# Kernel tuning notes

Measured on AMD Instinct MI355X. Metric: run time of the kernel, lower is better.

Reference implementation:

```python
import jax, jax.numpy as jnp
import numpy as np

D, B, E, O = 8, 16, 2048, 2048  # delays, batch, pre, post


def setup_inputs() -> dict:
    key = jax.random.key(0)
    k_w, k_mask, k_xd, k_dm, k_ws, k_sp = jax.random.split(key, 6)
    # W = connectivity mask * magnitudes (sparse non-negative weights, buffer wmax folded in)
    conn = jax.random.bernoulli(k_mask, 0.1, (E, O)).astype(jnp.float32)
    W = jax.random.uniform(k_w, (E, O), dtype=jnp.float32) * 0.02 * conn
    # Delayed presynaptic spikes: sparse binary
    Xd = jax.random.bernoulli(k_xd, 0.02, (D, B, E)).astype(jnp.float32)
    # delaymap: binary (delay, pre, post) routing map, typically ~1 active delay per synapse
    delaymap = jax.random.bernoulli(k_dm, 0.125, (D, E, O)).astype(jnp.float32)
    # STP modulation (output of shortterm module, before the +1 offset)
    Wshort = (jax.random.uniform(k_ws, (D, B, E), dtype=jnp.float32) - 0.5) * 0.4
    # Per-presynaptic-neuron signs in {-1,+1}, stored as int
    signs_pre = jax.random.randint(k_sp, (E,), 0, 2, dtype=jnp.int32)
    return {"W": W, "Xd": Xd, "delaymap": delaymap, "Wshort": Wshort,
            "signs_pre": signs_pre}


def reference(W, Xd, delaymap, Wshort, signs_pre):
    # align_signs(): signs = signs_pre broadcast over post, zeroed where W <= 0
    s = (2 * signs_pre - 1).astype(W.dtype)  # map {0,1} -> {-1,+1}
    signs = jnp.where(W > 0, s[:, None], jnp.zeros((), W.dtype))  # (E, O)
    Ws = signs * W  # signed weights 'eo'
    # has_STP path: I = einsum('eo,dbe,deo,dbe->bo', W, Xd, delaymap, Wshort+1)
    I = jnp.einsum('eo,dbe,deo,dbe->bo', Ws, Xd, delaymap, Wshort + 1.0)
    return I
```

## Files before the change

### kernel.cpp

```cpp
#include <hip/hip_runtime.h>


constexpr int D = 8, B = 16, E = 2048, O = 2048;
constexpr int DB = D * B;
constexpr int OTILE = 1024;
constexpr int THREADS2 = OTILE / 4;
constexpr int ESPLIT = 2;

struct Entry { int e; float c; };

__global__ __launch_bounds__(256) void build_lists(
    const float* __restrict__ Xd, const float* __restrict__ Wshort,
    const int* __restrict__ signs, int* __restrict__ counts,
    Entry* __restrict__ entries)
{
    const int db = blockIdx.x;
    __shared__ int cnt;
    if (threadIdx.x == 0) cnt = 0;
    __syncthreads();
    const float* xrow = Xd + (size_t)db * E;
    const float* wsr  = Wshort + (size_t)db * E;
    Entry* out = entries + (size_t)db * E;
    for (int e = threadIdx.x; e < E; e += blockDim.x) {
        float x = xrow[e];
        if (x != 0.0f) {
            float s = (float)(2 * signs[e] - 1);
            float c = x * s * (1.0f + wsr[e]);
            int slot = atomicAdd(&cnt, 1);
            out[slot].e = e;
            out[slot].c = c;
        }
    }
    __syncthreads();
    if (threadIdx.x == 0) counts[db] = cnt;
}

__global__ __launch_bounds__(THREADS2) void accum(
    const float* __restrict__ W, const float* __restrict__ dm,
    const int* __restrict__ counts, const Entry* __restrict__ entries,
    float* __restrict__ Iout)
{
    const int tile = blockIdx.x;
    const int part = blockIdx.y;
    const int db   = blockIdx.z;
    const int d = db / B;
    const int b = db % B;
    const int o0 = tile * OTILE + (int)threadIdx.x * 4;

    const int n = counts[db];
    const Entry* __restrict__ lst = entries + (size_t)db * E;

    float4 acc = make_float4(0.f, 0.f, 0.f, 0.f);
    #pragma unroll 2
    for (int i = part; i < n; i += ESPLIT) {
        Entry en = lst[i];
        const float4 w = *(const float4*)(W  + (size_t)en.e * O + o0);
        const float4 m = *(const float4*)(dm + ((size_t)d * E + en.e) * O + o0);
        acc.x += en.c * w.x * m.x;
        acc.y += en.c * w.y * m.y;
        acc.z += en.c * w.z * m.z;
        acc.w += en.c * w.w * m.w;
    }

    float* orow = Iout + (size_t)b * O + o0;
#if defined(__HIP_DEVICE_COMPILE__)
    unsafeAtomicAdd(orow + 0, acc.x);
    unsafeAtomicAdd(orow + 1, acc.y);
    unsafeAtomicAdd(orow + 2, acc.z);
    unsafeAtomicAdd(orow + 3, acc.w);
#endif
}

extern "C" void kernel_launch(void* const* d_in, const int* in_sizes, int n_in,
                              void* d_out, int out_size, void* d_ws, size_t ws_size,
                              hipStream_t stream) {
    const float* W     = (const float*)d_in[0];
    const float* Xd    = (const float*)d_in[1];
    const float* dm    = (const float*)d_in[2];
    const float* Wsh   = (const float*)d_in[3];
    const int*   signs = (const int*)d_in[4];
    float* Iout = (float*)d_out;

    int*   counts  = (int*)d_ws;
    Entry* entries = (Entry*)((char*)d_ws + 512);

    hipMemsetAsync(d_out, 0, sizeof(float) * (size_t)B * O, stream);
    build_lists<<<dim3(DB), dim3(256), 0, stream>>>(Xd, Wsh, signs, counts, entries);
    dim3 grid(O / OTILE, ESPLIT, DB);
    accum<<<grid, dim3(THREADS2), 0, stream>>>(W, dm, counts, entries, Iout);
}
```

Measured before the change: 200.8 us.

## Replace atomic accumulation with per-slice partials and a reduction kernel

```diff
diff --git a/kernel.cpp b/kernel.cpp
--- a/kernel.cpp
+++ b/kernel.cpp
@@ -3,9 +3,10 @@
 
 constexpr int D = 8, B = 16, E = 2048, O = 2048;
 constexpr int DB = D * B;
-constexpr int OTILE = 1024;
+constexpr int OTILE = 512;
 constexpr int THREADS2 = OTILE / 4;
-constexpr int ESPLIT = 2;
+constexpr int ESPLIT = 4;
+constexpr int NSLICE = D * ESPLIT;
 
 struct Entry { int e; float c; };
 
@@ -38,37 +39,50 @@
 __global__ __launch_bounds__(THREADS2) void accum(
     const float* __restrict__ W, const float* __restrict__ dm,
     const int* __restrict__ counts, const Entry* __restrict__ entries,
-    float* __restrict__ Iout)
+    float* __restrict__ partial)
 {
     const int tile = blockIdx.x;
     const int part = blockIdx.y;
     const int db   = blockIdx.z;
-    const int d = db / B;
-    const int b = db % B;
+    const int d = db >> 4;
+    const int b = db & 15;
     const int o0 = tile * OTILE + (int)threadIdx.x * 4;
 
     const int n = counts[db];
     const Entry* __restrict__ lst = entries + (size_t)db * E;
 
+    __shared__ Entry sh[E / ESPLIT];
+    for (int j = threadIdx.x; part + j * ESPLIT < n; j += THREADS2)
+        sh[j] = lst[part + j * ESPLIT];
+    const int m = (n - part + ESPLIT - 1) / ESPLIT;
+    __syncthreads();
+
+    const float* __restrict__ dmd = dm + (size_t)d * E * O;
     float4 acc = make_float4(0.f, 0.f, 0.f, 0.f);
-    #pragma unroll 2
-    for (int i = part; i < n; i += ESPLIT) {
-        Entry en = lst[i];
-        const float4 w = *(const float4*)(W  + (size_t)en.e * O + o0);
-        const float4 m = *(const float4*)(dm + ((size_t)d * E + en.e) * O + o0);
-        acc.x += en.c * w.x * m.x;
-        acc.y += en.c * w.y * m.y;
-        acc.z += en.c * w.z * m.z;
-        acc.w += en.c * w.w * m.w;
+    #pragma unroll 4
+    for (int j = 0; j < m; ++j) {
+        Entry en = sh[j];
+        const float4 w  = *(const float4*)(W   + (size_t)en.e * O + o0);
+        const float4 mm = *(const float4*)(dmd + (size_t)en.e * O + o0);
+        acc.x += en.c * w.x * mm.x;
+        acc.y += en.c * w.y * mm.y;
+        acc.z += en.c * w.z * mm.z;
+        acc.w += en.c * w.w * mm.w;
     }
 
-    float* orow = Iout + (size_t)b * O + o0;
-#if defined(__HIP_DEVICE_COMPILE__)
-    unsafeAtomicAdd(orow + 0, acc.x);
-    unsafeAtomicAdd(orow + 1, acc.y);
-    unsafeAtomicAdd(orow + 2, acc.z);
-    unsafeAtomicAdd(orow + 3, acc.w);
-#endif
+    float* p = partial + ((size_t)(d * ESPLIT + part) * B + b) * O + o0;
+    *(float4*)p = acc;
+}
+
+__global__ __launch_bounds__(256) void reduce_slices(
+    const float* __restrict__ partial, float* __restrict__ Iout)
+{
+    const int bo = blockIdx.x * 256 + threadIdx.x;
+    float s = 0.f;
+    #pragma unroll
+    for (int k = 0; k < NSLICE; ++k)
+        s += partial[(size_t)k * B * O + bo];
+    Iout[bo] = s;
 }
 
 extern "C" void kernel_launch(void* const* d_in, const int* in_sizes, int n_in,
@@ -83,9 +97,10 @@
 
     int*   counts  = (int*)d_ws;
     Entry* entries = (Entry*)((char*)d_ws + 512);
+    float* partial = (float*)((char*)d_ws + (4u << 20));
 
-    hipMemsetAsync(d_out, 0, sizeof(float) * (size_t)B * O, stream);
     build_lists<<<dim3(DB), dim3(256), 0, stream>>>(Xd, Wsh, signs, counts, entries);
     dim3 grid(O / OTILE, ESPLIT, DB);
-    accum<<<grid, dim3(THREADS2), 0, stream>>>(W, dm, counts, entries, Iout);
+    accum<<<grid, dim3(THREADS2), 0, stream>>>(W, dm, counts, entries, partial);
+    reduce_slices<<<dim3(B * O / 256), dim3(256), 0, stream>>>(partial, Iout);
 }
```

After: 198.5 us. No clear change (-1.1%).
